# Optimization experiments

Hardware: AMD Instinct MI355X
Metric: run time of the kernel (lower is better)

Reference implementation:

```python
import math
import jax, jax.numpy as jnp
import numpy as np

NUM_HEADS = 16


def setup_inputs() -> dict:
    key = jax.random.key(0)
    ks = jax.random.split(key, 5)
    B, S, H = 2, 2048, 1024
    hidden_states = jax.random.normal(ks[0], (B, S, H), dtype=jnp.float32)
    # causal lower-triangular float mask [1, 1, S, S], as the module expects
    ltor_mask = jnp.tril(jnp.ones((S, S), dtype=jnp.float32))[None, None, :, :]
    # weights stored pre-transposed: y = x @ W + b (equivalent to torch Linear)
    W_qkv = jax.random.normal(ks[1], (H, 3 * H), dtype=jnp.float32) * (1.0 / math.sqrt(H))
    b_qkv = jnp.zeros((3 * H,), dtype=jnp.float32)
    W_dense = jax.random.normal(ks[2], (H, H), dtype=jnp.float32) * (1.0 / math.sqrt(H))
    b_dense = jnp.zeros((H,), dtype=jnp.float32)
    return {
        "hidden_states": hidden_states,
        "ltor_mask": ltor_mask,
        "W_qkv": W_qkv,
        "b_qkv": b_qkv,
        "W_dense": W_dense,
        "b_dense": b_dense,
    }


def reference(hidden_states, ltor_mask, W_qkv, b_qkv, W_dense, b_dense):
    B, S, H = hidden_states.shape
    nh = NUM_HEADS
    hd = H // nh

    # fused QKV projection: [B, S, 3H] -> split -> [B, nh, S, hd]
    qkv = hidden_states @ W_qkv + b_qkv
    q, k, v = jnp.split(qkv, 3, axis=-1)

    def to_heads(x):
        return x.reshape(B, S, nh, hd).transpose(0, 2, 1, 3)

    q, k, v = to_heads(q), to_heads(k), to_heads(v)

    # scaled dot-product scores [B, nh, S, S]
    scores = jnp.einsum("bhqd,bhkd->bhqk", q, k) / math.sqrt(hd)
    # mul/sub causal masking, exactly as the torch module does
    scores = scores * ltor_mask - 10000.0 * (1.0 - ltor_mask)
    probs = jax.nn.softmax(scores, axis=-1)
    # attention dropout omitted (eval mode / p=0.0)

    ctx = jnp.einsum("bhqk,bhkd->bhqd", probs, v)
    ctx = ctx.transpose(0, 2, 1, 3).reshape(B, S, H)

    out = ctx @ W_dense + b_dense
    # output dropout omitted (eval mode / p=0.0)
    return out
```

## Files before the change

### kernel.cpp

```cpp
#include <hip/hip_runtime.h>
#include <math.h>

#define BATCH 2
#define SEQ   2048
#define HID   1024
#define NHEAD 16
#define HDIM  64
#define MTOT  (BATCH * SEQ)
#define QKVN  (3 * HID)
#define HBUF  ((size_t)BATCH * NHEAD * SEQ * HDIM)

typedef _Float16 f16x8 __attribute__((ext_vector_type(8)));
typedef _Float16 f16x4 __attribute__((ext_vector_type(4)));
typedef float    f32x4 __attribute__((ext_vector_type(4)));

#define MFMA16(a, b, c) __builtin_amdgcn_mfma_f32_16x16x32_f16((a), (b), (c), 0, 0, 0)

#define GLDS16(gp, lp) __builtin_amdgcn_global_load_lds( \
    (const __attribute__((address_space(1))) void*)(gp), \
    (__attribute__((address_space(3))) void*)(lp), 16, 0, 0)

#if __has_builtin(__builtin_amdgcn_exp2f)
#define EXP2F(x) __builtin_amdgcn_exp2f(x)
#else
#define EXP2F(x) exp2f(x)
#endif

#define SCALE2 0.18033688011f
#define MASK2  -14426.950408f
#define BIAS2  -4.0f

__global__ __launch_bounds__(256) void prep_kernel(
    const float* __restrict__ hs, const float* __restrict__ Wqkv,
    const float* __restrict__ Wd, _Float16* __restrict__ A_h,
    _Float16* __restrict__ outQ, _Float16* __restrict__ outD)
{
    __shared__ _Float16 T[32][36];
    const int gid = blockIdx.x;
    const int tid = threadIdx.x;
    if (gid < 2048) {
        const int ci = gid * 256 + tid;
        const int m = ci >> 7, cc = ci & 127;
        const int g = cc >> 2, c = cc & 3;
        const float* src = hs + (size_t)m * 1024 + cc * 8;
        f16x8 o;
#pragma unroll
        for (int j = 0; j < 8; ++j) o[j] = (_Float16)src[j];
        *(f16x8*)(A_h + (size_t)m * 1024 + g * 32 + ((c ^ (m & 3)) << 3)) = o;
        return;
    }
    const int tb = gid - 2048;
    const int bx = tb & 127, k0 = (tb >> 7) * 32;
    const float* in;
    _Float16* out;
    int N, n0;
    if (bx < 96) { in = Wqkv; out = outQ; N = QKVN; n0 = bx * 32; }
    else         { in = Wd;   out = outD; N = HID;  n0 = (bx - 96) * 32; }
    {
        const int r = tid >> 3, c4 = (tid & 7) * 4;
        float4 v = *(const float4*)(in + (size_t)(k0 + r) * N + n0 + c4);
        T[r][c4 + 0] = (_Float16)v.x;
        T[r][c4 + 1] = (_Float16)v.y;
        T[r][c4 + 2] = (_Float16)v.z;
        T[r][c4 + 3] = (_Float16)v.w;
    }
    __syncthreads();
    {
        const int nn = tid >> 3, k4 = (tid & 7) * 4;
        const int n = n0 + nn;
        f16x4 o;
        o[0] = T[k4 + 0][nn]; o[1] = T[k4 + 1][nn];
        o[2] = T[k4 + 2][nn]; o[3] = T[k4 + 3][nn];
        const int pos = ((k4 >> 3) ^ (n & 3)), half = (k4 >> 2) & 1;
        *(f16x4*)(out + (size_t)n * 1024 + k0 + pos * 8 + half * 4) = o;
    }
}

template<int EPI, int TM>
__global__ __launch_bounds__(256) void mfma_gemm(
    const _Float16* __restrict__ A, const _Float16* __restrict__ Bt,
    const float* __restrict__ bias, void* __restrict__ Cout,
    int M, int N, int K)
{
    __shared__ __align__(16) char SMEM[36864];
    _Float16* As = (_Float16*)SMEM;
    _Float16* Bs = As + TM * 32;
    constexpr int TI = TM / 32;
    constexpr int AR = TM / 4;

    const int tid = threadIdx.x;
    const int w = tid >> 6, l = tid & 63;
    const int a = l & 15, q4 = l >> 4;
    const int m0 = blockIdx.y * TM, n0 = blockIdx.x * 128;
    const int wm = (w >> 1) * (TM / 2), wn = (w & 1) * 64;

    f32x4 acc[TI][4];
#pragma unroll
    for (int i = 0; i < TI; ++i)
#pragma unroll
        for (int j = 0; j < 4; ++j) acc[i][j] = (f32x4){0.f, 0.f, 0.f, 0.f};

    const _Float16* gA = A + (size_t)(m0 + w * AR + (l >> 2)) * K + (l & 3) * 8;
    const _Float16* gB = Bt + (size_t)(n0 + w * 32 + (l >> 2)) * K + (l & 3) * 8;
    _Float16* sA = As + w * AR * 32;
    _Float16* sB = Bs + w * 1024;

    for (int k0 = 0; k0 < K; k0 += 32) {
#pragma unroll
        for (int u = 0; u < TM / 64; ++u)
            GLDS16(gA + (size_t)u * 16 * K + k0, sA + u * 512);
        GLDS16(gB + k0,          sB);
        GLDS16(gB + 16 * K + k0, sB + 512);
        __syncthreads();

        f16x8 af[TI], bf[4];
        const int pa = (q4 ^ (a & 3)) << 3;
#pragma unroll
        for (int i = 0; i < TI; ++i)
            af[i] = *(const f16x8*)&As[(wm + 16 * i + a) * 32 + pa];
#pragma unroll
        for (int j = 0; j < 4; ++j)
            bf[j] = *(const f16x8*)&Bs[(wn + 16 * j + a) * 32 + pa];
#pragma unroll
        for (int i = 0; i < TI; ++i)
#pragma unroll
            for (int j = 0; j < 4; ++j)
                acc[i][j] = MFMA16(af[i], bf[j], acc[i][j]);
        __syncthreads();
    }

    if (EPI == 0) {
        const int nbase = n0 + wn;
        const int t = nbase >> 10, h = (nbase >> 6) & 15;
        const int bb = (m0 + wm) >> 11;
        const int sbase = (m0 + wm) & 2047;
        _Float16* base = (_Float16*)Cout;
        _Float16* Cw = (_Float16*)SMEM + w * 4608;
        const int lsub = l >> 3, c = l & 7;
        if (t != 2) {
#pragma unroll
            for (int j = 0; j < 4; ++j) {
                const float bv = bias[nbase + 16 * j + a];
#pragma unroll
                for (int i = 0; i < 4; ++i)
#pragma unroll
                    for (int r = 0; r < 4; ++r)
                        Cw[(16 * i + q4 * 4 + r) * 72 + 16 * j + a] =
                            (_Float16)(acc[i][j][r] + bv);
            }
            const int cswz = (t == 1) ? (c ^ lsub) : c;
            _Float16* gq = base + (size_t)t * HBUF
                         + ((size_t)(bb * 16 + h) * 2048 + sbase) * 64;
#pragma unroll
            for (int pp = 0; pp < 8; ++pp) {
                const int lr = pp * 8 + lsub;
                f16x8 v8 = *(const f16x8*)&Cw[lr * 72 + cswz * 8];
                *(f16x8*)(gq + (size_t)lr * 64 + c * 8) = v8;
            }
        } else {
#pragma unroll
            for (int j = 0; j < 4; ++j) {
                const float bv = bias[nbase + 16 * j + a];
#pragma unroll
                for (int i = 0; i < 4; ++i) {
                    f16x4 pk;
#pragma unroll
                    for (int r = 0; r < 4; ++r)
                        pk[r] = (_Float16)(acc[i][j][r] + bv);
                    *(f16x4*)&Cw[(16 * j + a) * 72 + 16 * i + q4 * 4] = pk;
                }
            }
            const int cswz = c ^ lsub;
            _Float16* gv = base + 2 * HBUF
                         + ((size_t)(bb * 16 + h) * 64) * 2048 + sbase;
#pragma unroll
            for (int pp = 0; pp < 8; ++pp) {
                const int d = pp * 8 + lsub;
                f16x8 v8 = *(const f16x8*)&Cw[d * 72 + cswz * 8];
                *(f16x8*)(gv + (size_t)d * 2048 + c * 8) = v8;
            }
        }
    } else {
        float* C = (float*)Cout;
        float* Cw = (float*)SMEM + w * 2176;
#pragma unroll
        for (int j = 0; j < 4; ++j) {
            const float bv = bias[n0 + wn + 16 * j + a];
#pragma unroll
            for (int i = 0; i < TI; ++i)
#pragma unroll
                for (int r = 0; r < 4; ++r)
                    Cw[(16 * i + q4 * 4 + r) * 68 + 16 * j + a] =
                        acc[i][j][r] + bv;
        }
        const int lsub = l >> 4, c = l & 15;
        float* gout = C + (size_t)(m0 + wm) * N + n0 + wn;
#pragma unroll
        for (int pp = 0; pp < 8; ++pp) {
            const int lr = pp * 4 + lsub;
            float4 v4 = *(const float4*)&Cw[lr * 68 + c * 4];
            *(float4*)(gout + (size_t)lr * N + c * 4) = v4;
        }
    }
}

__global__ __launch_bounds__(256, 2) void attn_mfma(
    const _Float16* __restrict__ qb, const _Float16* __restrict__ kb,
    const _Float16* __restrict__ vtb, _Float16* __restrict__ ctx)
{
    __shared__ _Float16 Ks[2][64 * 64];
    __shared__ _Float16 VT[2][64 * 64];
    __shared__ _Float16 Ps[4][16 * 64];

    const int bid = blockIdx.x;
    const int jj = bid >> 3;
    const int bhIdx = (bid & 7) * 4 + (jj >> 4);
    const int p = jj & 15;
    const int b = bhIdx >> 4, h = bhIdx & 15;
    const int tid = threadIdx.x;
    const int w = tid >> 6, l = tid & 63;
    const int a = l & 15, q4 = l >> 4, a7 = a & 7;
    const size_t bh  = ((size_t)b * NHEAD + h) * SEQ;
    const size_t bhd = ((size_t)b * NHEAD + h) * 64;

    const int qHi = (31 - p) * 64 + w * 16;
    const int qLo = p * 64 + w * 16;
    const int ntiles = 32 - p;

    f16x8 qfh[2], qfl[2];
    {
        const _Float16* qp = qb + (bh + qHi + a) * 64;
        qfh[0] = *(const f16x8*)(qp + q4 * 8);
        qfh[1] = *(const f16x8*)(qp + 32 + q4 * 8);
        const _Float16* ql = qb + (bh + qLo + a) * 64;
        qfl[0] = *(const f16x8*)(ql + q4 * 8);
        qfl[1] = *(const f16x8*)(ql + 32 + q4 * 8);
    }

    f32x4 Oh[4], Ol[4];
#pragma unroll
    for (int c = 0; c < 4; ++c) {
        Oh[c] = (f32x4){0.f, 0.f, 0.f, 0.f};
        Ol[c] = (f32x4){0.f, 0.f, 0.f, 0.f};
    }
    float lh = 0.f, ll = 0.f;

    const _Float16* kg = kb + (bh + w * 16) * 64 + l * 8;
    const int vrow = w * 16 + (l >> 3);
    const _Float16* vg = vtb + (bhd + vrow) * 2048 + (l & 7) * 8;
    _Float16* pbuf = &Ps[w][0];
    const int p0 = (q4 ^ a7) << 3;

    auto stage = [&](int t, int buf) {
        _Float16* ksl = &Ks[buf][0] + w * 1024 + l * 8;
        const _Float16* kt = kg + (size_t)t * 4096;
        GLDS16(kt,       ksl);
        GLDS16(kt + 512, ksl + 512);
        _Float16* vtl = &VT[buf][0] + vrow * 64 + (l & 7) * 8;
        GLDS16(vg + t * 64,            vtl);
        GLDS16(vg + t * 64 + 8 * 2048, vtl + 512);
    };

    stage(0, 0);

    for (int t = 0; t < ntiles; ++t) {
        __syncthreads();
        if (t + 1 < ntiles) stage(t + 1, (t + 1) & 1);

        const _Float16* ksb  = &Ks[t & 1][0];
        const _Float16* vbuf = &VT[t & 1][0];
        const int kt0 = t * 64;
        const bool doLo = (t <= p);

        f32x4 sh[4], sl[4];
#pragma unroll
        for (int n0 = 0; n0 < 4; ++n0) {
            f16x8 kf0 = *(const f16x8*)&ksb[(n0 * 16 + a) * 64 + p0];
            f16x8 kf1 = *(const f16x8*)&ksb[(n0 * 16 + a) * 64 + (p0 ^ 32)];
            f32x4 c = (f32x4){0.f, 0.f, 0.f, 0.f};
            c = MFMA16(kf0, qfh[0], c);
            c = MFMA16(kf1, qfh[1], c);
            sh[n0] = c;
            if (doLo) {
                f32x4 d = (f32x4){0.f, 0.f, 0.f, 0.f};
                d = MFMA16(kf0, qfl[0], d);
                d = MFMA16(kf1, qfl[1], d);
                sl[n0] = d;
            }
        }

        auto half_step = [&](f32x4 st[4], float& lrun, f32x4* O,
                             const bool maskT, const int qbase) {
            if (maskT) {
#pragma unroll
                for (int n0 = 0; n0 < 4; ++n0)
#pragma unroll
                    for (int r = 0; r < 4; ++r) {
                        const int kgl = kt0 + n0 * 16 + q4 * 4 + r;
                        st[n0][r] = (kgl > qbase + a) ? MASK2
                                                      : fmaf(st[n0][r], SCALE2, BIAS2);
                    }
            } else {
#pragma unroll
                for (int n0 = 0; n0 < 4; ++n0)
#pragma unroll
                    for (int r = 0; r < 4; ++r)
                        st[n0][r] = fmaf(st[n0][r], SCALE2, BIAS2);
            }
            float ls = 0.f;
#pragma unroll
            for (int n0 = 0; n0 < 4; ++n0)
#pragma unroll
                for (int r = 0; r < 4; ++r) {
                    const float pe = EXP2F(st[n0][r]);
                    st[n0][r] = pe;
                    ls += pe;
                }
            lrun += ls;
#pragma unroll
            for (int n0 = 0; n0 < 4; ++n0) {
                f16x4 pk;
#pragma unroll
                for (int r = 0; r < 4; ++r) pk[r] = (_Float16)st[n0][r];
                const int pos = (2 * n0 + (q4 >> 1)) ^ a7;
                *(f16x4*)&pbuf[a * 64 + pos * 8 + ((q4 & 1) << 2)] = pk;
            }
            f16x8 pf0 = *(const f16x8*)&pbuf[a * 64 + p0];
            f16x8 pf1 = *(const f16x8*)&pbuf[a * 64 + (p0 ^ 32)];
#pragma unroll
            for (int c = 0; c < 4; ++c) {
                f16x8 vf0 = *(const f16x8*)&vbuf[(c * 16 + a) * 64 + p0];
                f16x8 vf1 = *(const f16x8*)&vbuf[(c * 16 + a) * 64 + (p0 ^ 32)];
                O[c] = MFMA16(vf0, pf0, O[c]);
                O[c] = MFMA16(vf1, pf1, O[c]);
            }
        };

        half_step(sh, lh, Oh, t == 31 - p, qHi);
        if (doLo) half_step(sl, ll, Ol, t == p, qLo);
    }

    auto finish = [&](float lrun, const f32x4* O, const int qbase) {
        float lt = lrun;
        lt += __shfl_xor(lt, 16);
        lt += __shfl_xor(lt, 32);
        const float inv = 1.0f / lt;
        const size_t row = (size_t)b * SEQ + qbase + a;
#pragma unroll
        for (int c = 0; c < 4; ++c) {
            const int d0 = c * 16 + q4 * 4;
            const int kcol = h * 64 + (d0 & ~31)
                           + ((((d0 >> 3) & 3) ^ (a & 3)) << 3) + (d0 & 7);
            f16x4 ov;
#pragma unroll
            for (int r = 0; r < 4; ++r) ov[r] = (_Float16)(O[c][r] * inv);
            *(f16x4*)(ctx + row * HID + kcol) = ov;
        }
    };
    finish(lh, Oh, qHi);
    finish(ll, Ol, qLo);
}

extern "C" void kernel_launch(void* const* d_in, const int* in_sizes, int n_in,
                              void* d_out, int out_size, void* d_ws, size_t ws_size,
                              hipStream_t stream) {
    const float* hs   = (const float*)d_in[0];
    const float* Wqkv = (const float*)d_in[2];
    const float* bqkv = (const float*)d_in[3];
    const float* Wd   = (const float*)d_in[4];
    const float* bd   = (const float*)d_in[5];

    _Float16* A_h   = (_Float16*)d_ws;
    _Float16* WqkvT = A_h + (size_t)MTOT * HID;
    _Float16* WdT   = WqkvT + (size_t)QKVN * HID;
    _Float16* qbuf  = WdT + (size_t)HID * HID;
    _Float16* ctxb  = qbuf + 3 * HBUF;

    prep_kernel<<<6144, 256, 0, stream>>>(hs, Wqkv, Wd, A_h, WqkvT, WdT);

    mfma_gemm<0, 128><<<dim3(QKVN / 128, MTOT / 128), 256, 0, stream>>>(
        A_h, WqkvT, bqkv, (void*)qbuf, MTOT, QKVN, HID);

    attn_mfma<<<512, 256, 0, stream>>>(
        qbuf, qbuf + HBUF, qbuf + 2 * HBUF, ctxb);

    mfma_gemm<1, 64><<<dim3(HID / 128, MTOT / 64), 256, 0, stream>>>(
        ctxb, WdT, bd, d_out, MTOT, HID, HID);
}
```

Measured before the change: 205.0 us.

## Shrink GEMM LDS footprint, stronger swizzle, and share V fragments across attention halves

Changes the LDS swizzle for the A/B GEMM operands (and the matching layout from prep and attention ctx writes) to XOR with two row bit-pairs, aiming to cut bank conflicts. Halves the GEMM shared memory by running the epilogue staging in two passes (or per-row-tile for the fp32 output), which should allow more resident blocks. In attention, softmax for the high and low query halves is computed first, then each V fragment is loaded once and used for both PV MFMAs, reducing LDS reads. The cost is more epilogue passes and higher register pressure in attention.

```diff
diff --git a/kernel.cpp b/kernel.cpp
--- a/kernel.cpp
+++ b/kernel.cpp
@@ -29,6 +29,8 @@
 #define SCALE2 0.18033688011f
 #define MASK2  -14426.950408f
 #define BIAS2  -4.0f
+
+#define SWZ4(row) (((row) & 3) ^ (((row) >> 2) & 3))
 
 __global__ __launch_bounds__(256) void prep_kernel(
     const float* __restrict__ hs, const float* __restrict__ Wqkv,
@@ -46,7 +48,7 @@
         f16x8 o;
 #pragma unroll
         for (int j = 0; j < 8; ++j) o[j] = (_Float16)src[j];
-        *(f16x8*)(A_h + (size_t)m * 1024 + g * 32 + ((c ^ (m & 3)) << 3)) = o;
+        *(f16x8*)(A_h + (size_t)m * 1024 + g * 32 + ((c ^ SWZ4(m)) << 3)) = o;
         return;
     }
     const int tb = gid - 2048;
@@ -71,7 +73,7 @@
         f16x4 o;
         o[0] = T[k4 + 0][nn]; o[1] = T[k4 + 1][nn];
         o[2] = T[k4 + 2][nn]; o[3] = T[k4 + 3][nn];
-        const int pos = ((k4 >> 3) ^ (n & 3)), half = (k4 >> 2) & 1;
+        const int pos = ((k4 >> 3) ^ SWZ4(n)), half = (k4 >> 2) & 1;
         *(f16x4*)(out + (size_t)n * 1024 + k0 + pos * 8 + half * 4) = o;
     }
 }
@@ -82,7 +84,8 @@
     const float* __restrict__ bias, void* __restrict__ Cout,
     int M, int N, int K)
 {
-    __shared__ __align__(16) char SMEM[36864];
+    constexpr int SMEM_BYTES = (EPI == 0) ? 18432 : 17408;
+    __shared__ __align__(16) char SMEM[SMEM_BYTES];
     _Float16* As = (_Float16*)SMEM;
     _Float16* Bs = As + TM * 32;
     constexpr int TI = TM / 32;
@@ -114,7 +117,7 @@
         __syncthreads();
 
         f16x8 af[TI], bf[4];
-        const int pa = (q4 ^ (a & 3)) << 3;
+        const int pa = (q4 ^ SWZ4(a)) << 3;
 #pragma unroll
         for (int i = 0; i < TI; ++i)
             af[i] = *(const f16x8*)&As[(wm + 16 * i + a) * 32 + pa];
@@ -135,71 +138,77 @@
         const int bb = (m0 + wm) >> 11;
         const int sbase = (m0 + wm) & 2047;
         _Float16* base = (_Float16*)Cout;
-        _Float16* Cw = (_Float16*)SMEM + w * 4608;
+        _Float16* Cw = (_Float16*)SMEM + w * 2304;
         const int lsub = l >> 3, c = l & 7;
         if (t != 2) {
-#pragma unroll
-            for (int j = 0; j < 4; ++j) {
-                const float bv = bias[nbase + 16 * j + a];
-#pragma unroll
-                for (int i = 0; i < 4; ++i)
-#pragma unroll
-                    for (int r = 0; r < 4; ++r)
-                        Cw[(16 * i + q4 * 4 + r) * 72 + 16 * j + a] =
-                            (_Float16)(acc[i][j][r] + bv);
-            }
             const int cswz = (t == 1) ? (c ^ lsub) : c;
             _Float16* gq = base + (size_t)t * HBUF
                          + ((size_t)(bb * 16 + h) * 2048 + sbase) * 64;
 #pragma unroll
-            for (int pp = 0; pp < 8; ++pp) {
-                const int lr = pp * 8 + lsub;
-                f16x8 v8 = *(const f16x8*)&Cw[lr * 72 + cswz * 8];
-                *(f16x8*)(gq + (size_t)lr * 64 + c * 8) = v8;
+            for (int pass = 0; pass < 2; ++pass) {
+#pragma unroll
+                for (int j = 0; j < 4; ++j) {
+                    const float bv = bias[nbase + 16 * j + a];
+#pragma unroll
+                    for (int i2 = 0; i2 < 2; ++i2)
+#pragma unroll
+                        for (int r = 0; r < 4; ++r)
+                            Cw[(16 * i2 + q4 * 4 + r) * 72 + 16 * j + a] =
+                                (_Float16)(acc[2 * pass + i2][j][r] + bv);
+                }
+#pragma unroll
+                for (int pp = 0; pp < 4; ++pp) {
+                    const int lr = pp * 8 + lsub;
+                    f16x8 v8 = *(const f16x8*)&Cw[lr * 72 + cswz * 8];
+                    *(f16x8*)(gq + (size_t)(32 * pass + lr) * 64 + c * 8) = v8;
+                }
             }
         } else {
-#pragma unroll
-            for (int j = 0; j < 4; ++j) {
-                const float bv = bias[nbase + 16 * j + a];
-#pragma unroll
-                for (int i = 0; i < 4; ++i) {
-                    f16x4 pk;
-#pragma unroll
-                    for (int r = 0; r < 4; ++r)
-                        pk[r] = (_Float16)(acc[i][j][r] + bv);
-                    *(f16x4*)&Cw[(16 * j + a) * 72 + 16 * i + q4 * 4] = pk;
-                }
-            }
             const int cswz = c ^ lsub;
             _Float16* gv = base + 2 * HBUF
                          + ((size_t)(bb * 16 + h) * 64) * 2048 + sbase;
 #pragma unroll
-            for (int pp = 0; pp < 8; ++pp) {
-                const int d = pp * 8 + lsub;
-                f16x8 v8 = *(const f16x8*)&Cw[d * 72 + cswz * 8];
-                *(f16x8*)(gv + (size_t)d * 2048 + c * 8) = v8;
+            for (int pass = 0; pass < 2; ++pass) {
+#pragma unroll
+                for (int jj = 0; jj < 2; ++jj) {
+                    const int j = 2 * pass + jj;
+                    const float bv = bias[nbase + 16 * j + a];
+#pragma unroll
+                    for (int i = 0; i < 4; ++i) {
+                        f16x4 pk;
+#pragma unroll
+                        for (int r = 0; r < 4; ++r)
+                            pk[r] = (_Float16)(acc[i][j][r] + bv);
+                        *(f16x4*)&Cw[(16 * jj + a) * 72 + 16 * i + q4 * 4] = pk;
+                    }
+                }
+#pragma unroll
+                for (int pp = 0; pp < 4; ++pp) {
+                    const int dl = pp * 8 + lsub;
+                    f16x8 v8 = *(const f16x8*)&Cw[dl * 72 + cswz * 8];
+                    *(f16x8*)(gv + (size_t)(32 * pass + dl) * 2048 + c * 8) = v8;
+                }
             }
         }
     } else {
         float* C = (float*)Cout;
-        float* Cw = (float*)SMEM + w * 2176;
-#pragma unroll
-        for (int j = 0; j < 4; ++j) {
-            const float bv = bias[n0 + wn + 16 * j + a];
-#pragma unroll
-            for (int i = 0; i < TI; ++i)
+        float* Cw = (float*)SMEM + w * 1088;
+        const int lr = l >> 2, lc = l & 3;
+#pragma unroll
+        for (int i = 0; i < TI; ++i) {
+#pragma unroll
+            for (int j = 0; j < 4; ++j) {
+                const float bv = bias[n0 + wn + 16 * j + a];
 #pragma unroll
                 for (int r = 0; r < 4; ++r)
-                    Cw[(16 * i + q4 * 4 + r) * 68 + 16 * j + a] =
-                        acc[i][j][r] + bv;
-        }
-        const int lsub = l >> 4, c = l & 15;
-        float* gout = C + (size_t)(m0 + wm) * N + n0 + wn;
-#pragma unroll
-        for (int pp = 0; pp < 8; ++pp) {
-            const int lr = pp * 4 + lsub;
-            float4 v4 = *(const float4*)&Cw[lr * 68 + c * 4];
-            *(float4*)(gout + (size_t)lr * N + c * 4) = v4;
+                    Cw[(q4 * 4 + r) * 68 + 16 * j + a] = acc[i][j][r] + bv;
+            }
+            float* gout = C + (size_t)(m0 + wm + 16 * i + lr) * N + n0 + wn;
+#pragma unroll
+            for (int pp = 0; pp < 4; ++pp) {
+                float4 v4 = *(const float4*)&Cw[lr * 68 + (lc + 4 * pp) * 4];
+                *(float4*)(gout + (lc + 4 * pp) * 4) = v4;
+            }
         }
     }
 }
@@ -289,8 +298,8 @@
             }
         }
 
-        auto half_step = [&](f32x4 st[4], float& lrun, f32x4* O,
-                             const bool maskT, const int qbase) {
+        auto softmax_P = [&](f32x4 st[4], float& lrun, const bool maskT,
+                             const int qbase, f16x8& pf0, f16x8& pf1) {
             if (maskT) {
 #pragma unroll
                 for (int n0 = 0; n0 < 4; ++n0)
@@ -325,19 +334,25 @@
                 const int pos = (2 * n0 + (q4 >> 1)) ^ a7;
                 *(f16x4*)&pbuf[a * 64 + pos * 8 + ((q4 & 1) << 2)] = pk;
             }
-            f16x8 pf0 = *(const f16x8*)&pbuf[a * 64 + p0];
-            f16x8 pf1 = *(const f16x8*)&pbuf[a * 64 + (p0 ^ 32)];
-#pragma unroll
-            for (int c = 0; c < 4; ++c) {
-                f16x8 vf0 = *(const f16x8*)&vbuf[(c * 16 + a) * 64 + p0];
-                f16x8 vf1 = *(const f16x8*)&vbuf[(c * 16 + a) * 64 + (p0 ^ 32)];
-                O[c] = MFMA16(vf0, pf0, O[c]);
-                O[c] = MFMA16(vf1, pf1, O[c]);
-            }
+            pf0 = *(const f16x8*)&pbuf[a * 64 + p0];
+            pf1 = *(const f16x8*)&pbuf[a * 64 + (p0 ^ 32)];
         };
 
-        half_step(sh, lh, Oh, t == 31 - p, qHi);
-        if (doLo) half_step(sl, ll, Ol, t == p, qLo);
+        f16x8 pfh0, pfh1, pfl0, pfl1;
+        softmax_P(sh, lh, t == 31 - p, qHi, pfh0, pfh1);
+        if (doLo) softmax_P(sl, ll, t == p, qLo, pfl0, pfl1);
+
+#pragma unroll
+        for (int c = 0; c < 4; ++c) {
+            f16x8 vf0 = *(const f16x8*)&vbuf[(c * 16 + a) * 64 + p0];
+            f16x8 vf1 = *(const f16x8*)&vbuf[(c * 16 + a) * 64 + (p0 ^ 32)];
+            Oh[c] = MFMA16(vf0, pfh0, Oh[c]);
+            Oh[c] = MFMA16(vf1, pfh1, Oh[c]);
+            if (doLo) {
+                Ol[c] = MFMA16(vf0, pfl0, Ol[c]);
+                Ol[c] = MFMA16(vf1, pfl1, Ol[c]);
+            }
+        }
     }
 
     auto finish = [&](float lrun, const f32x4* O, const int qbase) {
@@ -350,7 +365,7 @@
         for (int c = 0; c < 4; ++c) {
             const int d0 = c * 16 + q4 * 4;
             const int kcol = h * 64 + (d0 & ~31)
-                           + ((((d0 >> 3) & 3) ^ (a & 3)) << 3) + (d0 & 7);
+                           + ((((d0 >> 3) & 3) ^ SWZ4(a)) << 3) + (d0 & 7);
             f16x4 ov;
 #pragma unroll
             for (int r = 0; r < 4; ++r) ov[r] = (_Float16)(O[c][r] * inv);
```

After: 205.7 us. About the same (+0.4%).
